# Kernel optimization log

Measured on AMD Instinct MI355X. Metric: run time of the kernel, lower is better.

Reference implementation:

```python
import jax, jax.numpy as jnp
import numpy as np

N, E = 50000, 800000
DN, DE, H = 128, 64, 8
C = DN // H  # per-head dim = 16


def setup_inputs() -> dict:
    key = jax.random.key(0)
    ks = jax.random.split(key, 16)
    s = 0.05
    inp = {
        "node_state": jax.random.normal(ks[0], (N, DN), jnp.float32),
        "edge_index": jax.random.randint(ks[1], (2, E), 0, N, jnp.int64 if jax.config.jax_enable_x64 else jnp.int32),
        "edge_state": jax.random.normal(ks[2], (E, DE), jnp.float32),
        # edge_proj: Linear(DE, DE)
        "W_edge": jax.random.normal(ks[3], (DE, DE), jnp.float32) * s,
        "b_edge": jnp.zeros((DE,), jnp.float32),
        # TransformerConv linears (in, out) layout: y = x @ W + b
        "Wq": jax.random.normal(ks[4], (DN, DN), jnp.float32) * s,
        "bq": jnp.zeros((DN,), jnp.float32),
        "Wk": jax.random.normal(ks[5], (DN, DN), jnp.float32) * s,
        "bk": jnp.zeros((DN,), jnp.float32),
        "Wv": jax.random.normal(ks[6], (DN, DN), jnp.float32) * s,
        "bv": jnp.zeros((DN,), jnp.float32),
        "We": jax.random.normal(ks[7], (DE, DN), jnp.float32) * s,  # lin_edge, no bias
        "Wskip": jax.random.normal(ks[8], (DN, DN), jnp.float32) * s,
        "bskip": jnp.zeros((DN,), jnp.float32),
        "Wbeta": jax.random.normal(ks[9], (3 * DN, 1), jnp.float32) * s,  # lin_beta, no bias
        "ln_g": jnp.ones((DN,), jnp.float32),
        "ln_b": jnp.zeros((DN,), jnp.float32),
    }
    return inp


def reference(node_state, edge_index, edge_state, W_edge, b_edge, Wq, bq, Wk, bk,
              Wv, bv, We, Wskip, bskip, Wbeta, ln_g, ln_b):
    n = node_state.shape[0]
    src, dst = edge_index[0], edge_index[1]

    # edge_proj
    edge_attr = edge_state @ W_edge + b_edge  # [E, DE]

    # TransformerConv (beta=True, concat=True, dropout in eval mode)
    q = (node_state @ Wq + bq).reshape(n, H, C)
    k = (node_state @ Wk + bk).reshape(n, H, C)
    v = (node_state @ Wv + bv).reshape(n, H, C)
    e = (edge_attr @ We).reshape(-1, H, C)  # [E, H, C]

    kj = k[src] + e                                        # [E, H, C]
    alpha = jnp.sum(q[dst] * kj, axis=-1) / np.sqrt(C)     # [E, H]

    # segment softmax over destination nodes
    amax = jax.ops.segment_max(alpha, dst, num_segments=n)  # [N, H]
    ex = jnp.exp(alpha - amax[dst])
    denom = jax.ops.segment_sum(ex, dst, num_segments=n)    # [N, H]
    a = ex / denom[dst]                                     # [E, H]

    msg = (v[src] + e) * a[:, :, None]                      # [E, H, C]
    out = jax.ops.segment_sum(msg, dst, num_segments=n).reshape(n, DN)

    # beta-gated skip
    x_r = node_state @ Wskip + bskip
    beta = jax.nn.sigmoid(jnp.concatenate([out, x_r, out - x_r], axis=-1) @ Wbeta)  # [N, 1]
    out = beta * x_r + (1.0 - beta) * out

    # LayerNorm
    mu = jnp.mean(out, axis=-1, keepdims=True)
    var = jnp.mean(jnp.square(out - mu), axis=-1, keepdims=True)
    normed = (out - mu) * jax.lax.rsqrt(var + 1e-5) * ln_g + ln_b

    # residual + relu (dropout is identity in eval)
    return node_state + jax.nn.relu(normed)
```

## Files before the change

kernel.cpp:

```cpp
#include <hip/hip_runtime.h>
#include <cstdint>
#include <cstddef>

#define NN 50000
#define NE 800000

typedef short bf16x8 __attribute__((ext_vector_type(8)));
typedef float f32x4 __attribute__((ext_vector_type(4)));

__device__ __forceinline__ float b2f(unsigned short s) {
  union { unsigned int u; float f; } x; x.u = ((unsigned int)s) << 16; return x.f;
}
__device__ __forceinline__ unsigned short f2b(float f) {
  union { float f; unsigned int u; } x; x.f = f;
  unsigned int r = x.u + 0x7FFFu + ((x.u >> 16) & 1u);
  return (unsigned short)(r >> 16);
}

#define WS_WCE    0u
#define WS_BCE    16384u
#define WS_WCEF   20480u
#define WS_WALLF  40960u
#define WS_BALL   172032u
#define WS_QB     180224u
#define WS_KB     12980224u
#define WS_VB     25780224u
#define WS_XR     38580224u
#define WS_EB     64180224u
#define WS_CNT    268980224u
#define WS_OFF    269180224u
#define WS_CUR    269380224u
#define WS_BSUM   269580224u
#define WS_POS    269584320u
#define WS_SRCS   272784320u

__global__ void k_prep(const float* __restrict__ W_edge, const float* __restrict__ b_edge,
                       const float* __restrict__ We, unsigned short* __restrict__ wce,
                       float* __restrict__ bce) {
  int i = blockIdx.x;
  int j = threadIdx.x;
  float s = 0.f;
  for (int m = 0; m < 64; ++m) s += W_edge[i*64+m] * We[m*128+j];
  wce[i*128+j] = f2b(s);
  if (i == 0) {
    float bb = 0.f;
    for (int m = 0; m < 64; ++m) bb += b_edge[m] * We[m*128+j];
    bce[j] = bb;
  }
}

__global__ void k_pack_wce(const unsigned short* __restrict__ wce, unsigned short* __restrict__ wcef) {
  int fb = blockIdx.x;
  int ct = fb >> 1, s = fb & 1;
  int l = threadIdx.x;
  unsigned short* dst = wcef + (((size_t)(ct*2+s))*64 + l)*8;
  int col = ct*16 + (l & 15);
  int k0 = s*32 + (l >> 4)*8;
  #pragma unroll
  for (int j = 0; j < 8; ++j) dst[j] = wce[(k0+j)*128 + col];
}

__global__ void k_pack_wall(const float* __restrict__ Wq, const float* __restrict__ Wk,
                            const float* __restrict__ Wv, const float* __restrict__ Ws,
                            unsigned short* __restrict__ wallf) {
  int fb = blockIdx.x;
  int mat = fb >> 5, ct = (fb >> 2) & 7, s = fb & 3;
  int l = threadIdx.x;
  const float* W = (mat==0) ? Wq : (mat==1) ? Wk : (mat==2) ? Wv : Ws;
  unsigned short* dst = wallf + ((((size_t)(mat*8+ct))*4 + s)*64 + l)*8;
  int col = ct*16 + (l & 15);
  int k0 = s*32 + (l >> 4)*8;
  #pragma unroll
  for (int j = 0; j < 8; ++j) dst[j] = f2b(W[(k0+j)*128 + col]);
}

__global__ void k_pack_bias(const float* __restrict__ bq, const float* __restrict__ bk,
                            const float* __restrict__ bv, const float* __restrict__ bs,
                            float* __restrict__ ball) {
  int m = blockIdx.x, c = threadIdx.x;
  const float* b = (m==0) ? bq : (m==1) ? bk : (m==2) ? bv : bs;
  ball[m*128 + c] = b[c];
}

__global__ void __launch_bounds__(256) k_node_mfma(const float* __restrict__ x,
    const unsigned short* __restrict__ wallf, const float* __restrict__ ball,
    unsigned short* __restrict__ qb, unsigned short* __restrict__ kb,
    unsigned short* __restrict__ vb, float* __restrict__ xr) {
  __shared__ unsigned short sA[128*128];
  int mat = blockIdx.x & 3;
  int n0 = (blockIdx.x >> 2) * 128;
  for (int i = 0; i < 8; ++i) {
    int c = threadIdx.x + i*256;
    int row = c >> 4, ch = c & 15;
    int sw = (ch & 8) | ((ch & 7) ^ (row & 7));
    unsigned short tmp[8];
    if (n0 + row < NN) {
      const float* src = x + (size_t)(n0+row)*128 + ch*8;
      float4 f0 = *(const float4*)src;
      float4 f1 = *(const float4*)(src + 4);
      tmp[0]=f2b(f0.x); tmp[1]=f2b(f0.y); tmp[2]=f2b(f0.z); tmp[3]=f2b(f0.w);
      tmp[4]=f2b(f1.x); tmp[5]=f2b(f1.y); tmp[6]=f2b(f1.z); tmp[7]=f2b(f1.w);
    } else {
      #pragma unroll
      for (int j = 0; j < 8; ++j) tmp[j] = 0;
    }
    *(uint4*)&sA[row*128 + sw*8] = *(const uint4*)tmp;
  }
  __syncthreads();
  int l = threadIdx.x & 63, w = threadIdx.x >> 6;
  int g = l >> 4, ln = l & 15;
  f32x4 acc[2][8];
  #pragma unroll
  for (int rt = 0; rt < 2; ++rt)
    #pragma unroll
    for (int ct = 0; ct < 8; ++ct) acc[rt][ct] = (f32x4){0.f,0.f,0.f,0.f};
  for (int s = 0; s < 4; ++s) {
    bf16x8 wf[8];
    #pragma unroll
    for (int ct = 0; ct < 8; ++ct)
      wf[ct] = *(const bf16x8*)(wallf + ((((size_t)(mat*8+ct))*4 + s)*64 + l)*8);
    bf16x8 bfr[2];
    #pragma unroll
    for (int rt = 0; rt < 2; ++rt) {
      int row = w*32 + rt*16 + ln;
      int ch = s*4 + g;
      int sw = (ch & 8) | ((ch & 7) ^ (row & 7));
      bfr[rt] = *(const bf16x8*)&sA[row*128 + sw*8];
    }
    #pragma unroll
    for (int rt = 0; rt < 2; ++rt)
      #pragma unroll
      for (int ct = 0; ct < 8; ++ct)
        acc[rt][ct] = __builtin_amdgcn_mfma_f32_16x16x32_bf16(wf[ct], bfr[rt], acc[rt][ct], 0, 0, 0);
  }
  #pragma unroll
  for (int rt = 0; rt < 2; ++rt) {
    int node = n0 + w*32 + rt*16 + ln;
    if (node >= NN) continue;
    #pragma unroll
    for (int ct = 0; ct < 8; ++ct) {
      int c0 = ct*16 + g*4;
      float4 bi = *(const float4*)(ball + mat*128 + c0);
      float v0 = acc[rt][ct][0] + bi.x, v1 = acc[rt][ct][1] + bi.y;
      float v2 = acc[rt][ct][2] + bi.z, v3 = acc[rt][ct][3] + bi.w;
      if (mat == 3) {
        float4 o = {v0, v1, v2, v3};
        *(float4*)(xr + (size_t)node*128 + c0) = o;
      } else {
        unsigned short* dst = (mat==0) ? qb : (mat==1) ? kb : vb;
        unsigned short o[4] = {f2b(v0), f2b(v1), f2b(v2), f2b(v3)};
        *(uint2*)(dst + (size_t)node*128 + c0) = *(const uint2*)o;
      }
    }
  }
}

__global__ void __launch_bounds__(256) k_egemm_mfma(const float* __restrict__ es,
    const unsigned short* __restrict__ wcef, const float* __restrict__ bce,
    const int* __restrict__ pos, unsigned short* __restrict__ eb) {
  __shared__ unsigned short sA[128*64];
  __shared__ unsigned short sO[128*128];
  int e0 = blockIdx.x * 128;
  for (int i = 0; i < 4; ++i) {
    int c = threadIdx.x + i*256;
    int row = c >> 3, ch = c & 7;
    int sw = ch ^ (row & 7);
    const float* src = es + (size_t)(e0+row)*64 + ch*8;
    float4 f0 = *(const float4*)src;
    float4 f1 = *(const float4*)(src + 4);
    unsigned short tmp[8];
    tmp[0]=f2b(f0.x); tmp[1]=f2b(f0.y); tmp[2]=f2b(f0.z); tmp[3]=f2b(f0.w);
    tmp[4]=f2b(f1.x); tmp[5]=f2b(f1.y); tmp[6]=f2b(f1.z); tmp[7]=f2b(f1.w);
    *(uint4*)&sA[row*64 + sw*8] = *(const uint4*)tmp;
  }
  __syncthreads();
  int l = threadIdx.x & 63, w = threadIdx.x >> 6;
  int g = l >> 4, ln = l & 15;
  f32x4 acc[2][8];
  #pragma unroll
  for (int rt = 0; rt < 2; ++rt)
    #pragma unroll
    for (int ct = 0; ct < 8; ++ct) acc[rt][ct] = (f32x4){0.f,0.f,0.f,0.f};
  #pragma unroll
  for (int s = 0; s < 2; ++s) {
    bf16x8 wf[8];
    #pragma unroll
    for (int ct = 0; ct < 8; ++ct)
      wf[ct] = *(const bf16x8*)(wcef + (((size_t)(ct*2+s))*64 + l)*8);
    bf16x8 bfr[2];
    #pragma unroll
    for (int rt = 0; rt < 2; ++rt) {
      int row = w*32 + rt*16 + ln;
      int ch = (s*4 + g) ^ (row & 7);
      bfr[rt] = *(const bf16x8*)&sA[row*64 + ch*8];
    }
    #pragma unroll
    for (int rt = 0; rt < 2; ++rt)
      #pragma unroll
      for (int ct = 0; ct < 8; ++ct)
        acc[rt][ct] = __builtin_amdgcn_mfma_f32_16x16x32_bf16(wf[ct], bfr[rt], acc[rt][ct], 0, 0, 0);
  }
  #pragma unroll
  for (int rt = 0; rt < 2; ++rt) {
    int row = w*32 + rt*16 + ln;
    #pragma unroll
    for (int ct = 0; ct < 8; ++ct) {
      int c0 = ct*16 + g*4;
      float4 bi = *(const float4*)(bce + c0);
      unsigned short o[4] = {f2b(acc[rt][ct][0]+bi.x), f2b(acc[rt][ct][1]+bi.y),
                             f2b(acc[rt][ct][2]+bi.z), f2b(acc[rt][ct][3]+bi.w)};
      int ch = ct*2 + (g >> 1);
      int sw = (ch & 8) | ((ch & 7) ^ (row & 7));
      *(uint2*)&sO[row*128 + sw*8 + (g & 1)*4] = *(const uint2*)o;
    }
  }
  __syncthreads();
  int rrow = threadIdx.x >> 4;
  int rch  = threadIdx.x & 15;
  #pragma unroll
  for (int it = 0; it < 8; ++it) {
    int r = it*16 + rrow;
    int sw = (rch & 8) | ((rch & 7) ^ (r & 7));
    uint4 val = *(const uint4*)&sO[r*128 + sw*8];
    int prow = pos[e0 + r];
    *(uint4*)(eb + (size_t)prow*128 + rch*8) = val;
  }
}

__global__ void __launch_bounds__(256) k_hist(const int* __restrict__ ei, int* __restrict__ cnt) {
  int t = blockIdx.x * 256 + threadIdx.x;
  if (t < NE) atomicAdd(&cnt[ei[NE + t]], 1);
}

__global__ void __launch_bounds__(256) k_scanA(const int* __restrict__ cnt,
    int* __restrict__ off, int* __restrict__ bsum) {
  __shared__ int s[256];
  int i = blockIdx.x * 256 + threadIdx.x;
  int v = (i < NN) ? cnt[i] : 0;
  s[threadIdx.x] = v;
  __syncthreads();
  #pragma unroll
  for (int d = 1; d < 256; d <<= 1) {
    int t = (threadIdx.x >= d) ? s[threadIdx.x - d] : 0;
    __syncthreads();
    s[threadIdx.x] += t;
    __syncthreads();
  }
  if (i < NN) off[i] = s[threadIdx.x] - v;
  if (threadIdx.x == 255) bsum[blockIdx.x] = s[255];
}

__global__ void __launch_bounds__(256) k_scanB(int* __restrict__ bsum, int nb) {
  __shared__ int s[256];
  int v = (threadIdx.x < nb) ? bsum[threadIdx.x] : 0;
  s[threadIdx.x] = v;
  __syncthreads();
  #pragma unroll
  for (int d = 1; d < 256; d <<= 1) {
    int t = (threadIdx.x >= d) ? s[threadIdx.x - d] : 0;
    __syncthreads();
    s[threadIdx.x] += t;
    __syncthreads();
  }
  if (threadIdx.x < nb) bsum[threadIdx.x] = s[threadIdx.x] - v;
}

__global__ void __launch_bounds__(256) k_scanC(int* __restrict__ off,
    const int* __restrict__ bsum, int* __restrict__ cur) {
  int i = blockIdx.x * 256 + threadIdx.x;
  if (i < NN) {
    int o = off[i] + bsum[blockIdx.x];
    off[i] = o;
    cur[i] = o;
  }
}

__global__ void __launch_bounds__(256) k_scatter(const int* __restrict__ ei,
    int* __restrict__ cur, int* __restrict__ pos, int* __restrict__ srcs) {
  int t = blockIdx.x * 256 + threadIdx.x;
  if (t < NE) {
    int d = ei[NE + t];
    int p = atomicAdd(&cur[d], 1);
    pos[t] = p;
    srcs[p] = ei[t];
  }
}

__global__ void __launch_bounds__(256) k_attn(
    const int* __restrict__ off, const int* __restrict__ cnt,
    const int* __restrict__ srcs,
    const unsigned short* __restrict__ qb, const unsigned short* __restrict__ kb,
    const unsigned short* __restrict__ vb, const unsigned short* __restrict__ eb,
    const float* __restrict__ xr, const float* __restrict__ x,
    const float* __restrict__ Wb, const float* __restrict__ ln_g,
    const float* __restrict__ ln_b, float* __restrict__ out) {
  int wid = threadIdx.x >> 6, lane = threadIdx.x & 63;
  int n = blockIdx.x * 4 + wid;
  if (n >= NN) return;
  int c = lane * 2;

  unsigned int qu = *(const unsigned int*)(qb + (size_t)n*128 + c);
  float q0 = b2f((unsigned short)(qu & 0xffffu)), q1 = b2f((unsigned short)(qu >> 16));

  int start = off[n], m = cnt[n];
  const int* sp = srcs + start;
  const unsigned short* ep = eb + (size_t)start*128 + c;
  float acc0 = 0.f, acc1 = 0.f, den = 0.f;

  auto body = [&](unsigned int ku, unsigned int eu, unsigned int vu) {
    float e0 = b2f((unsigned short)(eu & 0xffffu)), e1 = b2f((unsigned short)(eu >> 16));
    float p = q0*(b2f((unsigned short)(ku & 0xffffu)) + e0)
            + q1*(b2f((unsigned short)(ku >> 16)) + e1);
    p += __shfl_xor(p, 1);
    p += __shfl_xor(p, 2);
    p += __shfl_xor(p, 4);
    float a = __expf(p * 0.25f);
    den  += a;
    acc0 += a * (b2f((unsigned short)(vu & 0xffffu)) + e0);
    acc1 += a * (b2f((unsigned short)(vu >> 16)) + e1);
  };

  int i = 0;
  for (; i + 2 <= m; i += 2) {
    int sA = sp[i], sB = sp[i+1];
    unsigned int euA = *(const unsigned int*)(ep + (size_t)i*128);
    unsigned int euB = *(const unsigned int*)(ep + (size_t)(i+1)*128);
    unsigned int kuA = *(const unsigned int*)(kb + (size_t)sA*128 + c);
    unsigned int vuA = *(const unsigned int*)(vb + (size_t)sA*128 + c);
    unsigned int kuB = *(const unsigned int*)(kb + (size_t)sB*128 + c);
    unsigned int vuB = *(const unsigned int*)(vb + (size_t)sB*128 + c);
    body(kuA, euA, vuA);
    body(kuB, euB, vuB);
  }
  if (i < m) {
    int sA = sp[i];
    unsigned int euA = *(const unsigned int*)(ep + (size_t)i*128);
    unsigned int kuA = *(const unsigned int*)(kb + (size_t)sA*128 + c);
    unsigned int vuA = *(const unsigned int*)(vb + (size_t)sA*128 + c);
    body(kuA, euA, vuA);
  }

  float inv = (m > 0) ? 1.f / den : 0.f;
  float o0 = acc0 * inv, o1 = acc1 * inv;

  float2 r = *(const float2*)(xr + (size_t)n*128 + c);
  float p = o0*Wb[c] + o1*Wb[c+1] + r.x*Wb[128+c] + r.y*Wb[128+c+1]
          + (o0-r.x)*Wb[256+c] + (o1-r.y)*Wb[256+c+1];
  #pragma unroll
  for (int offs = 32; offs > 0; offs >>= 1) p += __shfl_xor(p, offs);
  float beta = 1.f / (1.f + __expf(-p));
  float g0 = beta*r.x + (1.f-beta)*o0;
  float g1 = beta*r.y + (1.f-beta)*o1;
  float msum = g0 + g1;
  #pragma unroll
  for (int offs = 32; offs > 0; offs >>= 1) msum += __shfl_xor(msum, offs);
  msum *= (1.f/128.f);
  float d0 = g0 - msum, d1 = g1 - msum;
  float vv = d0*d0 + d1*d1;
  #pragma unroll
  for (int offs = 32; offs > 0; offs >>= 1) vv += __shfl_xor(vv, offs);
  vv *= (1.f/128.f);
  float rs = rsqrtf(vv + 1e-5f);
  float n0 = d0*rs*ln_g[c]   + ln_b[c];
  float n1 = d1*rs*ln_g[c+1] + ln_b[c+1];
  float2 xv = *(const float2*)(x + (size_t)n*128 + c);
  float2 res;
  res.x = xv.x + fmaxf(n0, 0.f);
  res.y = xv.y + fmaxf(n1, 0.f);
  *(float2*)(out + (size_t)n*128 + c) = res;
}

extern "C" void kernel_launch(void* const* d_in, const int* in_sizes, int n_in,
                              void* d_out, int out_size, void* d_ws, size_t ws_size,
                              hipStream_t stream) {
  const float* node   = (const float*)d_in[0];
  const int*   ei     = (const int*)  d_in[1];
  const float* es     = (const float*)d_in[2];
  const float* W_edge = (const float*)d_in[3];
  const float* b_edge = (const float*)d_in[4];
  const float* Wq     = (const float*)d_in[5];
  const float* bq     = (const float*)d_in[6];
  const float* Wk     = (const float*)d_in[7];
  const float* bk     = (const float*)d_in[8];
  const float* Wv     = (const float*)d_in[9];
  const float* bv     = (const float*)d_in[10];
  const float* We     = (const float*)d_in[11];
  const float* Wskip  = (const float*)d_in[12];
  const float* bskip  = (const float*)d_in[13];
  const float* Wbeta  = (const float*)d_in[14];
  const float* ln_g   = (const float*)d_in[15];
  const float* ln_b   = (const float*)d_in[16];

  char* ws = (char*)d_ws;
  unsigned short* wce   = (unsigned short*)(ws + WS_WCE);
  float*          bce   = (float*)(ws + WS_BCE);
  unsigned short* wcef  = (unsigned short*)(ws + WS_WCEF);
  unsigned short* wallf = (unsigned short*)(ws + WS_WALLF);
  float*          ball  = (float*)(ws + WS_BALL);
  unsigned short* qb  = (unsigned short*)(ws + WS_QB);
  unsigned short* kb  = (unsigned short*)(ws + WS_KB);
  unsigned short* vb  = (unsigned short*)(ws + WS_VB);
  float*          xr  = (float*)(ws + WS_XR);
  unsigned short* eb  = (unsigned short*)(ws + WS_EB);
  int*            cnt = (int*)(ws + WS_CNT);
  int*            off = (int*)(ws + WS_OFF);
  int*            cur = (int*)(ws + WS_CUR);
  int*            bsm = (int*)(ws + WS_BSUM);
  int*            pos = (int*)(ws + WS_POS);
  int*            srcs= (int*)(ws + WS_SRCS);

  hipMemsetAsync(cnt, 0, (size_t)NN*4, stream);

  k_prep<<<64, 128, 0, stream>>>(W_edge, b_edge, We, wce, bce);
  k_pack_wce<<<16, 64, 0, stream>>>(wce, wcef);
  k_pack_wall<<<128, 64, 0, stream>>>(Wq, Wk, Wv, Wskip, wallf);
  k_pack_bias<<<4, 128, 0, stream>>>(bq, bk, bv, bskip, ball);

  const int nbScan = (NN + 255)/256;
  k_hist<<<(NE + 255)/256, 256, 0, stream>>>(ei, cnt);
  k_scanA<<<nbScan, 256, 0, stream>>>(cnt, off, bsm);
  k_scanB<<<1, 256, 0, stream>>>(bsm, nbScan);
  k_scanC<<<nbScan, 256, 0, stream>>>(off, bsm, cur);
  k_scatter<<<(NE + 255)/256, 256, 0, stream>>>(ei, cur, pos, srcs);

  const int ntiles = (NN + 127) / 128;
  k_node_mfma<<<ntiles*4, 256, 0, stream>>>(node, wallf, ball, qb, kb, vb, xr);
  k_egemm_mfma<<<NE/128, 256, 0, stream>>>(es, wcef, bce, pos, eb);

  k_attn<<<(NN + 3)/4, 256, 0, stream>>>(off, cnt, srcs, qb, kb, vb, eb,
                                         xr, node, Wbeta, ln_g, ln_b, (float*)d_out);
}
```

Measured before the change: 350.4 us.

## Fuse attention scores and v+e into edge GEMM epilogue; stream them in aggregation

The edge GEMM epilogue now gathers q[dst], k[src] and v[src] for each edge. It computes the exponentiated per-head scores and the v+e message, then writes both in destination-sorted order. The aggregation kernel then only streams contiguous score and message rows instead of gathering k and v through a sorted src list, and the srcs array is dropped. In exchange the epilogue does more scattered, narrow gathers (now including q per edge) and writes an extra per-edge score buffer.

```diff
diff --git a/kernel.cpp b/kernel.cpp
--- a/kernel.cpp
+++ b/kernel.cpp
@@ -26,13 +26,13 @@
 #define WS_KB     12980224u
 #define WS_VB     25780224u
 #define WS_XR     38580224u
-#define WS_EB     64180224u
+#define WS_VEB    64180224u
 #define WS_CNT    268980224u
 #define WS_OFF    269180224u
 #define WS_CUR    269380224u
 #define WS_BSUM   269580224u
 #define WS_POS    269584320u
-#define WS_SRCS   272784320u
+#define WS_EX     272784320u
 
 __global__ void k_prep(const float* __restrict__ W_edge, const float* __restrict__ b_edge,
                        const float* __restrict__ We, unsigned short* __restrict__ wce,
@@ -157,7 +157,10 @@
 
 __global__ void __launch_bounds__(256) k_egemm_mfma(const float* __restrict__ es,
     const unsigned short* __restrict__ wcef, const float* __restrict__ bce,
-    const int* __restrict__ pos, unsigned short* __restrict__ eb) {
+    const int* __restrict__ pos, const int* __restrict__ ei,
+    const unsigned short* __restrict__ qb, const unsigned short* __restrict__ kb,
+    const unsigned short* __restrict__ vb,
+    unsigned short* __restrict__ veb, float* __restrict__ ex) {
   __shared__ unsigned short sA[128*64];
   __shared__ unsigned short sO[128*128];
   int e0 = blockIdx.x * 128;
@@ -203,16 +206,44 @@
   #pragma unroll
   for (int rt = 0; rt < 2; ++rt) {
     int row = w*32 + rt*16 + ln;
+    int t = e0 + row;
+    int src = ei[t];
+    int dstn = ei[NE + t];
+    float alo = 0.f, ahi = 0.f;
+    int hbase = g*2;
     #pragma unroll
     for (int ct = 0; ct < 8; ++ct) {
       int c0 = ct*16 + g*4;
       float4 bi = *(const float4*)(bce + c0);
-      unsigned short o[4] = {f2b(acc[rt][ct][0]+bi.x), f2b(acc[rt][ct][1]+bi.y),
-                             f2b(acc[rt][ct][2]+bi.z), f2b(acc[rt][ct][3]+bi.w)};
+      float e0v = acc[rt][ct][0] + bi.x;
+      float e1v = acc[rt][ct][1] + bi.y;
+      float e2v = acc[rt][ct][2] + bi.z;
+      float e3v = acc[rt][ct][3] + bi.w;
+      uint2 qu = *(const uint2*)(qb + (size_t)dstn*128 + c0);
+      uint2 ku = *(const uint2*)(kb + (size_t)src*128 + c0);
+      float part =
+          b2f((unsigned short)(qu.x & 0xffffu))*(b2f((unsigned short)(ku.x & 0xffffu))+e0v)
+        + b2f((unsigned short)(qu.x >> 16))    *(b2f((unsigned short)(ku.x >> 16))+e1v)
+        + b2f((unsigned short)(qu.y & 0xffffu))*(b2f((unsigned short)(ku.y & 0xffffu))+e2v)
+        + b2f((unsigned short)(qu.y >> 16))    *(b2f((unsigned short)(ku.y >> 16))+e3v);
+      part += __shfl_xor(part, 16);
+      part += __shfl_xor(part, 32);
+      float aval = __expf(part * 0.25f);
+      alo = (ct == hbase)     ? aval : alo;
+      ahi = (ct == hbase + 1) ? aval : ahi;
+      uint2 vu = *(const uint2*)(vb + (size_t)src*128 + c0);
+      unsigned short o[4] = {
+        f2b(b2f((unsigned short)(vu.x & 0xffffu))+e0v),
+        f2b(b2f((unsigned short)(vu.x >> 16))    +e1v),
+        f2b(b2f((unsigned short)(vu.y & 0xffffu))+e2v),
+        f2b(b2f((unsigned short)(vu.y >> 16))    +e3v)};
       int ch = ct*2 + (g >> 1);
       int sw = (ch & 8) | ((ch & 7) ^ (row & 7));
       *(uint2*)&sO[row*128 + sw*8 + (g & 1)*4] = *(const uint2*)o;
     }
+    int prow = pos[t];
+    float2 av = {alo, ahi};
+    *(float2*)(ex + (size_t)prow*8 + hbase) = av;
   }
   __syncthreads();
   int rrow = threadIdx.x >> 4;
@@ -223,7 +254,7 @@
     int sw = (rch & 8) | ((rch & 7) ^ (r & 7));
     uint4 val = *(const uint4*)&sO[r*128 + sw*8];
     int prow = pos[e0 + r];
-    *(uint4*)(eb + (size_t)prow*128 + rch*8) = val;
+    *(uint4*)(veb + (size_t)prow*128 + rch*8) = val;
   }
 }
 
@@ -276,68 +307,50 @@
 }
 
 __global__ void __launch_bounds__(256) k_scatter(const int* __restrict__ ei,
-    int* __restrict__ cur, int* __restrict__ pos, int* __restrict__ srcs) {
+    int* __restrict__ cur, int* __restrict__ pos) {
   int t = blockIdx.x * 256 + threadIdx.x;
   if (t < NE) {
     int d = ei[NE + t];
     int p = atomicAdd(&cur[d], 1);
     pos[t] = p;
-    srcs[p] = ei[t];
   }
 }
 
 __global__ void __launch_bounds__(256) k_attn(
     const int* __restrict__ off, const int* __restrict__ cnt,
-    const int* __restrict__ srcs,
-    const unsigned short* __restrict__ qb, const unsigned short* __restrict__ kb,
-    const unsigned short* __restrict__ vb, const unsigned short* __restrict__ eb,
+    const float* __restrict__ ex, const unsigned short* __restrict__ veb,
     const float* __restrict__ xr, const float* __restrict__ x,
     const float* __restrict__ Wb, const float* __restrict__ ln_g,
     const float* __restrict__ ln_b, float* __restrict__ out) {
   int wid = threadIdx.x >> 6, lane = threadIdx.x & 63;
   int n = blockIdx.x * 4 + wid;
   if (n >= NN) return;
-  int c = lane * 2;
-
-  unsigned int qu = *(const unsigned int*)(qb + (size_t)n*128 + c);
-  float q0 = b2f((unsigned short)(qu & 0xffffu)), q1 = b2f((unsigned short)(qu >> 16));
+  int c = lane * 2, h = lane >> 3;
 
   int start = off[n], m = cnt[n];
-  const int* sp = srcs + start;
-  const unsigned short* ep = eb + (size_t)start*128 + c;
+  const float* ap = ex + (size_t)start*8 + h;
+  const unsigned short* vp = veb + (size_t)start*128 + c;
   float acc0 = 0.f, acc1 = 0.f, den = 0.f;
 
-  auto body = [&](unsigned int ku, unsigned int eu, unsigned int vu) {
-    float e0 = b2f((unsigned short)(eu & 0xffffu)), e1 = b2f((unsigned short)(eu >> 16));
-    float p = q0*(b2f((unsigned short)(ku & 0xffffu)) + e0)
-            + q1*(b2f((unsigned short)(ku >> 16)) + e1);
-    p += __shfl_xor(p, 1);
-    p += __shfl_xor(p, 2);
-    p += __shfl_xor(p, 4);
-    float a = __expf(p * 0.25f);
-    den  += a;
-    acc0 += a * (b2f((unsigned short)(vu & 0xffffu)) + e0);
-    acc1 += a * (b2f((unsigned short)(vu >> 16)) + e1);
-  };
-
   int i = 0;
-  for (; i + 2 <= m; i += 2) {
-    int sA = sp[i], sB = sp[i+1];
-    unsigned int euA = *(const unsigned int*)(ep + (size_t)i*128);
-    unsigned int euB = *(const unsigned int*)(ep + (size_t)(i+1)*128);
-    unsigned int kuA = *(const unsigned int*)(kb + (size_t)sA*128 + c);
-    unsigned int vuA = *(const unsigned int*)(vb + (size_t)sA*128 + c);
-    unsigned int kuB = *(const unsigned int*)(kb + (size_t)sB*128 + c);
-    unsigned int vuB = *(const unsigned int*)(vb + (size_t)sB*128 + c);
-    body(kuA, euA, vuA);
-    body(kuB, euB, vuB);
-  }
-  if (i < m) {
-    int sA = sp[i];
-    unsigned int euA = *(const unsigned int*)(ep + (size_t)i*128);
-    unsigned int kuA = *(const unsigned int*)(kb + (size_t)sA*128 + c);
-    unsigned int vuA = *(const unsigned int*)(vb + (size_t)sA*128 + c);
-    body(kuA, euA, vuA);
+  for (; i + 4 <= m; i += 4) {
+    float a0 = ap[(i+0)*8], a1 = ap[(i+1)*8], a2 = ap[(i+2)*8], a3 = ap[(i+3)*8];
+    unsigned int u0 = *(const unsigned int*)(vp + (i+0)*128);
+    unsigned int u1 = *(const unsigned int*)(vp + (i+1)*128);
+    unsigned int u2 = *(const unsigned int*)(vp + (i+2)*128);
+    unsigned int u3 = *(const unsigned int*)(vp + (i+3)*128);
+    acc0 += a0*b2f((unsigned short)(u0 & 0xffffu)); acc1 += a0*b2f((unsigned short)(u0 >> 16));
+    acc0 += a1*b2f((unsigned short)(u1 & 0xffffu)); acc1 += a1*b2f((unsigned short)(u1 >> 16));
+    acc0 += a2*b2f((unsigned short)(u2 & 0xffffu)); acc1 += a2*b2f((unsigned short)(u2 >> 16));
+    acc0 += a3*b2f((unsigned short)(u3 & 0xffffu)); acc1 += a3*b2f((unsigned short)(u3 >> 16));
+    den += a0 + a1 + a2 + a3;
+  }
+  for (; i < m; ++i) {
+    float a = ap[i*8];
+    unsigned int u = *(const unsigned int*)(vp + (size_t)i*128);
+    acc0 += a*b2f((unsigned short)(u & 0xffffu));
+    acc1 += a*b2f((unsigned short)(u >> 16));
+    den += a;
   }
 
   float inv = (m > 0) ? 1.f / den : 0.f;
@@ -401,13 +414,13 @@
   unsigned short* kb  = (unsigned short*)(ws + WS_KB);
   unsigned short* vb  = (unsigned short*)(ws + WS_VB);
   float*          xr  = (float*)(ws + WS_XR);
-  unsigned short* eb  = (unsigned short*)(ws + WS_EB);
+  unsigned short* veb = (unsigned short*)(ws + WS_VEB);
   int*            cnt = (int*)(ws + WS_CNT);
   int*            off = (int*)(ws + WS_OFF);
   int*            cur = (int*)(ws + WS_CUR);
   int*            bsm = (int*)(ws + WS_BSUM);
   int*            pos = (int*)(ws + WS_POS);
-  int*            srcs= (int*)(ws + WS_SRCS);
+  float*          ex  = (float*)(ws + WS_EX);
 
   hipMemsetAsync(cnt, 0, (size_t)NN*4, stream);
 
@@ -421,12 +434,12 @@
   k_scanA<<<nbScan, 256, 0, stream>>>(cnt, off, bsm);
   k_scanB<<<1, 256, 0, stream>>>(bsm, nbScan);
   k_scanC<<<nbScan, 256, 0, stream>>>(off, bsm, cur);
-  k_scatter<<<(NE + 255)/256, 256, 0, stream>>>(ei, cur, pos, srcs);
+  k_scatter<<<(NE + 255)/256, 256, 0, stream>>>(ei, cur, pos);
 
   const int ntiles = (NN + 127) / 128;
   k_node_mfma<<<ntiles*4, 256, 0, stream>>>(node, wallf, ball, qb, kb, vb, xr);
-  k_egemm_mfma<<<NE/128, 256, 0, stream>>>(es, wcef, bce, pos, eb);
-
-  k_attn<<<(NN + 3)/4, 256, 0, stream>>>(off, cnt, srcs, qb, kb, vb, eb,
-                                         xr, node, Wbeta, ln_g, ln_b, (float*)d_out);
-}
+  k_egemm_mfma<<<NE/128, 256, 0, stream>>>(es, wcef, bce, pos, ei, qb, kb, vb, veb, ex);
+
+  k_attn<<<(NN + 3)/4, 256, 0, stream>>>(off, cnt, ex, veb, xr, node,
+                                         Wbeta, ln_g, ln_b, (float*)d_out);
+}
```

Measured after the change: 421.0 us. +20.1%, slower.
